# Performance work log

Hardware: AMD Instinct MI355X
Metric: run time of the kernel (lower is better)

The kernel has to match this reference:

```python
import jax, jax.numpy as jnp
import numpy as np

N_NODES = 100000
N_EDGES = 1600000
N_GRAPHS = 4096
GN_EPS = 1e-5
SLOPE = 0.01  # torch leaky_relu default negative_slope


def _graph_norm(x, w, b, s):
    # PyG GraphNorm with batch=None: single-graph normalization over all nodes
    mean = jnp.mean(x, axis=0, keepdims=True)
    out = x - s * mean
    var = jnp.mean(out * out, axis=0, keepdims=True)
    return w * out * jax.lax.rsqrt(var + GN_EPS) + b


def setup_inputs() -> dict:
    key = jax.random.key(0)
    ks = jax.random.split(key, 12)

    def rn(k, shape, fan_in):
        return (jax.random.normal(k, shape, jnp.float32) / np.float32(np.sqrt(fan_in)))

    return {
        "x": jax.random.normal(ks[0], (N_NODES, 48), jnp.float32),
        "edge_attr": jax.random.normal(ks[1], (N_EDGES, 10), jnp.float32),
        # GINConv MLP layer 0: Linear(48->128); layers 1..3: Linear(128->128)
        "W1_0": rn(ks[2], (48, 128), 48), "b1_0": jnp.zeros((128,), jnp.float32),
        "W1_rest": rn(ks[3], (3, 128, 128), 128), "b1_rest": jnp.zeros((3, 128), jnp.float32),
        # GraphNorm inside each MLP (weight, bias, mean_scale)
        "gn_w": jnp.ones((4, 128), jnp.float32), "gn_b": jnp.zeros((4, 128), jnp.float32), "gn_s": jnp.ones((4, 128), jnp.float32),
        # second Linear of each MLP (128->128; last conv maps to out_channels=128)
        "W2": rn(ks[4], (4, 128, 128), 128), "b2": jnp.zeros((4, 128), jnp.float32),
        # BasicGNN post-conv GraphNorms (after layers 0..2 only)
        "pn_w": jnp.ones((3, 128), jnp.float32), "pn_b": jnp.zeros((3, 128), jnp.float32), "pn_s": jnp.ones((3, 128), jnp.float32),
        # readout MLP head
        "fc1_W": rn(ks[5], (384, 64), 384), "fc1_b": jnp.zeros((64,), jnp.float32),
        "fc2_W": rn(ks[6], (64, 3), 64), "fc2_b": jnp.zeros((3,), jnp.float32),
        "edge_index": jax.random.randint(ks[7], (2, N_EDGES), 0, N_NODES),
        "batch": jnp.sort(jax.random.randint(ks[8], (N_NODES,), 0, N_GRAPHS)),
    }


def reference(x, edge_attr, W1_0, b1_0, W1_rest, b1_rest, gn_w, gn_b, gn_s,
              W2, b2, pn_w, pn_b, pn_s, fc1_W, fc1_b, fc2_W, fc2_b,
              edge_index, batch):
    # edge_attr is ignored: PyG GIN does not support edge attributes.
    src, dst = edge_index[0], edge_index[1]
    h = x
    for i in range(4):
        # GINConv: mlp((1+eps)*x_i + sum_{j in N(i)} x_j), eps = 0
        agg = jax.ops.segment_sum(h[src], dst, num_segments=N_NODES)
        m = h + agg
        if i == 0:
            m = m @ W1_0 + b1_0
        else:
            m = m @ W1_rest[i - 1] + b1_rest[i - 1]
        m = _graph_norm(m, gn_w[i], gn_b[i], gn_s[i])  # norm inside MLP
        m = jax.nn.leaky_relu(m, SLOPE)
        h = m @ W2[i] + b2[i]
        if i < 3:  # BasicGNN: norm + act after every conv except the last
            h = _graph_norm(h, pn_w[i], pn_b[i], pn_s[i])
            h = jax.nn.leaky_relu(h, SLOPE)

    # global mean / add / max pooling over data.batch
    sums = jax.ops.segment_sum(h, batch, num_segments=N_GRAPHS)
    cnt = jax.ops.segment_sum(jnp.ones((h.shape[0], 1), h.dtype), batch,
                              num_segments=N_GRAPHS)
    mean = sums / jnp.maximum(cnt, 1.0)
    mx = jax.ops.segment_max(h, batch, num_segments=N_GRAPHS)
    mx = jnp.where(jnp.isfinite(mx), mx, 0.0)  # guard empty segments

    g = jnp.concatenate([mean, sums, mx], axis=1)  # [G, 384]
    g = jax.nn.leaky_relu(g @ fc1_W + fc1_b, SLOPE)
    return g @ fc2_W + fc2_b  # [G, 3]
```

## Files before the change

kernel.cpp:

```cpp
#include <hip/hip_runtime.h>
#include <hip/hip_bf16.h>
#include <math.h>

#define N_NODES  100000
#define N_EDGES  1600000
#define N_GRAPHS 4096
#define NBUCKET  ((N_NODES + 127) / 128)
#define NPART    256
#define ROWBLKS_AL 6256

typedef __attribute__((ext_vector_type(4))) float f32x4;
typedef __attribute__((ext_vector_type(8))) short bf16x8;

__device__ __forceinline__ float lrelu(float x) { return fmaxf(x, 0.01f * x); }

__device__ __forceinline__ unsigned short f2bf(float f) {
    unsigned u = __float_as_uint(f);
    unsigned r = (u + 0x7FFFu + ((u >> 16) & 1u)) >> 16;
    return (unsigned short)r;
}
__device__ __forceinline__ float bf2f(unsigned short h) {
    return __uint_as_float(((unsigned)h) << 16);
}

__global__ __launch_bounds__(1024) void scan_kernel(const unsigned* __restrict__ in,
                                                    unsigned* __restrict__ out, int n) {
    __shared__ unsigned wsum[16];
    __shared__ unsigned carry_s;
    int t = threadIdx.x, lane = t & 63, wv = t >> 6;
    if (t == 0) carry_s = 0u;
    __syncthreads();
    for (int base = 0; base < n; base += 4096) {
        unsigned carry = carry_s;
        unsigned v[4]; unsigned s = 0u;
#pragma unroll
        for (int i = 0; i < 4; ++i) {
            int idx = base + t * 4 + i;
            v[i] = (idx < n) ? in[idx] : 0u;
            s += v[i];
        }
        unsigned ps = s;
#pragma unroll
        for (int off = 1; off < 64; off <<= 1) {
            unsigned x = __shfl_up(ps, off, 64);
            if (lane >= off) ps += x;
        }
        if (lane == 63) wsum[wv] = ps;
        __syncthreads();
        if (wv == 0 && lane < 16) {
            unsigned pw = wsum[lane];
#pragma unroll
            for (int off = 1; off < 16; off <<= 1) {
                unsigned x = __shfl_up(pw, off, 64);
                if (lane >= off) pw += x;
            }
            wsum[lane] = pw;
        }
        __syncthreads();
        unsigned wbase = wv ? wsum[wv - 1] : 0u;
        unsigned run = carry + wbase + (ps - s);
#pragma unroll
        for (int i = 0; i < 4; ++i) {
            int idx = base + t * 4 + i;
            if (idx < n) out[idx] = run;
            run += v[i];
        }
        unsigned total = wsum[15];
        __syncthreads();
        if (t == 0) carry_s = carry + total;
        __syncthreads();
    }
    if (t == 0) out[n] = carry_s;
}

__global__ __launch_bounds__(256) void phist_kernel(const int* __restrict__ dst,
        unsigned* __restrict__ cnt, int E, int chunk) {
    __shared__ unsigned lc[NBUCKET];
    int p = blockIdx.x, t = threadIdx.x;
    for (int i = t; i < NBUCKET; i += 256) lc[i] = 0u;
    __syncthreads();
    int e0 = p * chunk, e1 = e0 + chunk; if (e1 > E) e1 = E;
    for (int e = e0 + t; e < e1; e += 256)
        atomicAdd(&lc[((unsigned)dst[e]) >> 7], 1u);
    __syncthreads();
    for (int i = t; i < NBUCKET; i += 256) cnt[(size_t)p * NBUCKET + i] = lc[i];
}

__global__ void btot_kernel(const unsigned* __restrict__ cnt, unsigned* __restrict__ tot) {
    int b = blockIdx.x * 256 + threadIdx.x;
    if (b >= NBUCKET) return;
    unsigned s = 0u;
    for (int p = 0; p < NPART; ++p) s += cnt[(size_t)p * NBUCKET + b];
    tot[b] = s;
}

__global__ __launch_bounds__(256) void poff_kernel(unsigned* __restrict__ cnt,
        const unsigned* __restrict__ bucket_base) {
    int b = blockIdx.x * 4 + (threadIdx.x >> 6);
    if (b >= NBUCKET) return;
    int lane = threadIdx.x & 63;
    unsigned v[4]; unsigned s = 0u;
#pragma unroll
    for (int i = 0; i < 4; ++i) {
        int p = lane * 4 + i;
        v[i] = cnt[(size_t)p * NBUCKET + b];
        s += v[i];
    }
    unsigned ps = s;
#pragma unroll
    for (int off = 1; off < 64; off <<= 1) {
        unsigned x = __shfl_up(ps, off, 64);
        if (lane >= off) ps += x;
    }
    unsigned run = bucket_base[b] + (ps - s);
#pragma unroll
    for (int i = 0; i < 4; ++i) {
        int p = lane * 4 + i;
        cnt[(size_t)p * NBUCKET + b] = run;
        run += v[i];
    }
}

__global__ __launch_bounds__(256) void pscat_kernel(const int* __restrict__ ei,
        const unsigned* __restrict__ cnt, unsigned* __restrict__ pair, int E, int chunk) {
    __shared__ unsigned lcur[NBUCKET];
    int p = blockIdx.x, t = threadIdx.x;
    for (int i = t; i < NBUCKET; i += 256) lcur[i] = cnt[(size_t)p * NBUCKET + i];
    __syncthreads();
    int e0 = p * chunk, e1 = e0 + chunk; if (e1 > E) e1 = E;
    for (int e = e0 + t; e < e1; e += 256) {
        unsigned src = (unsigned)ei[e];
        unsigned dst = (unsigned)ei[E + e];
        unsigned b = dst >> 7;
        unsigned pos = atomicAdd(&lcur[b], 1u);
        pair[pos] = src | ((dst & 127u) << 20);
    }
}

__global__ __launch_bounds__(256) void fillc2_kernel(const unsigned* __restrict__ pair,
        const unsigned* __restrict__ bucket_base, unsigned* __restrict__ row_ptr,
        unsigned* __restrict__ col, int N) {
    __shared__ unsigned lcnt[128], lpre[128], lcur[128];
    int b = blockIdx.x;
    int node0 = b << 7;
    int t = threadIdx.x;
    if (t < 128) { lcnt[t] = 0u; lcur[t] = 0u; }
    __syncthreads();
    unsigned bb = bucket_base[b], be = bucket_base[b + 1];
    for (unsigned i = bb + t; i < be; i += 256)
        atomicAdd(&lcnt[(pair[i] >> 20) & 127u], 1u);
    __syncthreads();
    if (t < 64) {
        unsigned v0 = lcnt[2 * t], v1 = lcnt[2 * t + 1];
        unsigned s = v0 + v1;
        unsigned ps = s;
#pragma unroll
        for (int off = 1; off < 64; off <<= 1) {
            unsigned x = __shfl_up(ps, off, 64);
            if (t >= off) ps += x;
        }
        unsigned base = ps - s;
        lpre[2 * t] = base;
        lpre[2 * t + 1] = base + v0;
    }
    __syncthreads();
    if (t < 128) {
        int node = node0 + t;
        if (node < N) row_ptr[node] = bb + lpre[t];
    }
    if (b == (int)gridDim.x - 1 && t == 0) row_ptr[N] = be;
    for (unsigned i = bb + t; i < be; i += 256) {
        unsigned u = pair[i];
        unsigned d = (u >> 20) & 127u;
        unsigned pos = bb + lpre[d] + atomicAdd(&lcur[d], 1u);
        col[pos] = u & 0xFFFFFu;
    }
}

__global__ void gsearch_kernel(const int* __restrict__ batch, unsigned* __restrict__ gptr,
                               int N, int G) {
    int g = blockIdx.x * 256 + threadIdx.x;
    if (g > G) return;
    int lo = 0, hi = N;
    while (lo < hi) { int mid = (lo + hi) >> 1; if (batch[mid] < g) lo = mid + 1; else hi = mid; }
    gptr[g] = (unsigned)lo;
}

__global__ void cast_kernel(const float* __restrict__ in, unsigned short* __restrict__ outb, int n4) {
    int i = blockIdx.x * 256 + threadIdx.x;
    if (i >= n4) return;
    f32x4 v = *(const f32x4*)(in + (size_t)i * 4);
    uint2 u;
    u.x = (unsigned)f2bf(v[0]) | ((unsigned)f2bf(v[1]) << 16);
    u.y = (unsigned)f2bf(v[2]) | ((unsigned)f2bf(v[3]) << 16);
    *(uint2*)(outb + (size_t)i * 4) = u;
}

__global__ __launch_bounds__(256) void tfm_kernel(const unsigned short* __restrict__ hb,
        const float* __restrict__ stats, const float* __restrict__ wp,
        const float* __restrict__ bp, const float* __restrict__ sp, float invN,
        unsigned short* __restrict__ yb, int total8) {
    __shared__ float la[128], ldd[128];
    int t = threadIdx.x;
    if (t < 128) {
        float mean = stats[t] * invN;
        float ex2  = stats[128 + t] * invN;
        float sv   = sp[t];
        float var  = ex2 - 2.f * sv * mean * mean + sv * sv * mean * mean;
        float a    = wp[t] * rsqrtf(var + 1e-5f);
        la[t] = a; ldd[t] = bp[t] - a * sv * mean;
    }
    __syncthreads();
    int i = blockIdx.x * 256 + t;
    if (i >= total8) return;
    int c0 = (i & 15) * 8;
    uint4 u = *(const uint4*)(hb + (size_t)i * 8);
    unsigned uu[4] = {u.x, u.y, u.z, u.w};
    unsigned ow[4];
#pragma unroll
    for (int q = 0; q < 4; ++q) {
        int c = c0 + 2 * q;
        float v0 = lrelu(fmaf(la[c],     __uint_as_float(uu[q] << 16),         ldd[c]));
        float v1 = lrelu(fmaf(la[c + 1], __uint_as_float(uu[q] & 0xffff0000u), ldd[c + 1]));
        ow[q] = (unsigned)f2bf(v0) | ((unsigned)f2bf(v1) << 16);
    }
    uint4 o; o.x = ow[0]; o.y = ow[1]; o.z = ow[2]; o.w = ow[3];
    *(uint4*)(yb + (size_t)i * 8) = o;
}

template<int D, int KOCT>
__global__ __launch_bounds__(256) void agg_kernel(const unsigned short* __restrict__ hb, int ld_in,
        const unsigned* __restrict__ row_ptr, const unsigned* __restrict__ col,
        unsigned short* __restrict__ op, int n) {
    int node = blockIdx.x * 4 + (threadIdx.x >> 6);
    int l = threadIdx.x & 63;
    if (node >= n || l >= KOCT * 4) return;
    int c = 2 * l;
    float x0 = 0.f, x1 = 0.f;
    if (c < D) {
        const unsigned short* hp = hb + c;
#define LOADU(s) *(const unsigned*)(hp + (size_t)(s) * ld_in)
#define LO(u) __uint_as_float((u) << 16)
#define HI(u) __uint_as_float((u) & 0xffff0000u)
        unsigned su = LOADU(node);
        x0 = LO(su); x1 = HI(su);
        float y0 = 0.f, y1 = 0.f, z0 = 0.f, z1 = 0.f, q0 = 0.f, q1 = 0.f;
        unsigned e0 = row_ptr[node], e1 = row_ptr[node + 1];
        unsigned e = e0;
        for (; e + 8 <= e1; e += 8) {
            unsigned c0i = col[e],     c1i = col[e + 1], c2i = col[e + 2], c3i = col[e + 3];
            unsigned c4i = col[e + 4], c5i = col[e + 5], c6i = col[e + 6], c7i = col[e + 7];
            unsigned u0 = LOADU(c0i), u1 = LOADU(c1i), u2 = LOADU(c2i), u3 = LOADU(c3i);
            unsigned u4 = LOADU(c4i), u5 = LOADU(c5i), u6 = LOADU(c6i), u7 = LOADU(c7i);
            x0 += LO(u0); x1 += HI(u0); y0 += LO(u1); y1 += HI(u1);
            z0 += LO(u2); z1 += HI(u2); q0 += LO(u3); q1 += HI(u3);
            x0 += LO(u4); x1 += HI(u4); y0 += LO(u5); y1 += HI(u5);
            z0 += LO(u6); z1 += HI(u6); q0 += LO(u7); q1 += HI(u7);
        }
        for (; e + 4 <= e1; e += 4) {
            unsigned c0i = col[e], c1i = col[e + 1], c2i = col[e + 2], c3i = col[e + 3];
            unsigned u0 = LOADU(c0i), u1 = LOADU(c1i), u2 = LOADU(c2i), u3 = LOADU(c3i);
            x0 += LO(u0); x1 += HI(u0); y0 += LO(u1); y1 += HI(u1);
            z0 += LO(u2); z1 += HI(u2); q0 += LO(u3); q1 += HI(u3);
        }
        for (; e < e1; ++e) {
            unsigned u = LOADU(col[e]);
            x0 += LO(u); x1 += HI(u);
        }
#undef LOADU
#undef LO
#undef HI
        x0 = (x0 + y0) + (z0 + q0);
        x1 = (x1 + y1) + (z1 + q1);
    }
    unsigned outw = (unsigned)f2bf(x0) | ((unsigned)f2bf(x1) << 16);
    size_t fo = (((size_t)(node >> 4) * KOCT + (l >> 2)) * 16 + (node & 15)) * 8 + 2 * (l & 3);
    *(unsigned*)(op + fo) = outw;
}

__global__ __launch_bounds__(256) void wsplit_kernel(const float* __restrict__ W1_0,
        const float* __restrict__ W1_rest, const float* __restrict__ W2,
        unsigned short* __restrict__ wt) {
    int g = blockIdx.y;
    int i = blockIdx.x * 256 + threadIdx.x;
    int e = i & 7, lane = (i >> 3) & 63, h = (i >> 9) & 1, j = (i >> 10) & 7, ks = i >> 13;
    int m = lane & 15, kg = lane >> 4;
    int k = ks * 32 + kg * 8 + e;
    int n = 8 * m + j;
    float v = 0.f;
    if (g == 0) { if (k < 48) v = W1_0[k * 128 + n]; }
    else if (g & 1) v = W2[(size_t)((g - 1) >> 1) * 16384 + k * 128 + n];
    else            v = W1_rest[(size_t)((g - 2) >> 1) * 16384 + k * 128 + n];
    unsigned short hi = f2bf(v);
    unsigned short out = (h == 0) ? hi : f2bf(v - bf2f(hi));
    wt[(size_t)g * 32768 + i] = out;
}

template<int KS, int KOCT, bool AFF, bool STATS, bool BF16OUT, bool FRAGOUT>
__global__ __launch_bounds__(256, 2) void mgemm_kernel(
        const unsigned short* __restrict__ Ah,
        const float* __restrict__ stats, const float* __restrict__ wp,
        const float* __restrict__ bp, const float* __restrict__ sp, float invN,
        const unsigned short* __restrict__ Wt, const float* __restrict__ bias,
        unsigned short* __restrict__ outb, unsigned short* __restrict__ ofh,
        float* __restrict__ ostats, int M) {
    __shared__ float ls[256];
    int t = threadIdx.x;
    if (STATS) { ls[t] = 0.f; __syncthreads(); }
    int lane = t & 63;
    int m = lane & 15, kg = lane >> 4;
    int wid = t >> 6;
    int wr = wid >> 1, wc = wid & 1;
    int rowBase = blockIdx.x * 128 + wr * 64;
    int rowblk0 = blockIdx.x * 8 + wr * 4;

    union U8 { bf16x8 v; unsigned short u[8]; };

    f32x4 acc[4][4];
#pragma unroll
    for (int j = 0; j < 4; ++j) {
        float b = bias[8 * m + wc * 4 + j];
#pragma unroll
        for (int rg = 0; rg < 4; ++rg) acc[rg][j] = (f32x4){b, b, b, b};
    }

#pragma unroll
    for (int ks = 0; ks < KS; ++ks) {
        int k0 = ks * 32 + kg * 8;
        float aC[8], dC[8];
        if (AFF) {
            f32x4 sm0 = *(const f32x4*)(stats + k0),       sm1 = *(const f32x4*)(stats + k0 + 4);
            f32x4 se0 = *(const f32x4*)(stats + 128 + k0), se1 = *(const f32x4*)(stats + 128 + k0 + 4);
            f32x4 w0  = *(const f32x4*)(wp + k0),          w1  = *(const f32x4*)(wp + k0 + 4);
            f32x4 b0  = *(const f32x4*)(bp + k0),          b1  = *(const f32x4*)(bp + k0 + 4);
            f32x4 s0  = *(const f32x4*)(sp + k0),          s1  = *(const f32x4*)(sp + k0 + 4);
#pragma unroll
            for (int q = 0; q < 8; ++q) {
                float mean = (q < 4 ? sm0[q] : sm1[q - 4]) * invN;
                float ex2  = (q < 4 ? se0[q] : se1[q - 4]) * invN;
                float sv   = (q < 4 ? s0[q]  : s1[q - 4]);
                float var  = ex2 - 2.f * sv * mean * mean + sv * sv * mean * mean;
                float a    = (q < 4 ? w0[q] : w1[q - 4]) * rsqrtf(var + 1e-5f);
                aC[q] = a;
                dC[q] = (q < 4 ? b0[q] : b1[q - 4]) - a * sv * mean;
            }
        }
        U8 fh[4];
#pragma unroll
        for (int rg = 0; rg < 4; ++rg) {
            size_t ao = (((size_t)(rowblk0 + rg) * KOCT + ks * 4 + kg) << 7) + (m << 3);
            U8 h;
            h.v = *(const bf16x8*)(Ah + ao);
            if (AFF) {
#pragma unroll
                for (int q = 0; q < 8; ++q) {
                    float xv = lrelu(fmaf(aC[q], bf2f(h.u[q]), dC[q]));
                    h.u[q] = f2bf(xv);
                }
            }
            fh[rg] = h;
        }
#pragma unroll
        for (int j = 0; j < 4; ++j) {
            size_t wo = (size_t)(ks * 8 + wc * 4 + j) * 1024 + (size_t)lane * 8;
            bf16x8 whi = *(const bf16x8*)(Wt + wo);
            bf16x8 wlo = *(const bf16x8*)(Wt + wo + 512);
#pragma unroll
            for (int rg = 0; rg < 4; ++rg) {
                acc[rg][j] = __builtin_amdgcn_mfma_f32_16x16x32_bf16(fh[rg].v, whi, acc[rg][j], 0, 0, 0);
                acc[rg][j] = __builtin_amdgcn_mfma_f32_16x16x32_bf16(fh[rg].v, wlo, acc[rg][j], 0, 0, 0);
            }
        }
    }

#pragma unroll
    for (int rg = 0; rg < 4; ++rg) {
#pragma unroll
        for (int r = 0; r < 4; ++r) {
            int gr = rowBase + rg * 16 + kg * 4 + r;
            if (gr < M) {
                unsigned short h[4];
#pragma unroll
                for (int q = 0; q < 4; ++q) h[q] = f2bf(acc[rg][q][r]);
                uint2 uh;
                uh.x = (unsigned)h[0] | ((unsigned)h[1] << 16);
                uh.y = (unsigned)h[2] | ((unsigned)h[3] << 16);
                if (BF16OUT) *(uint2*)(outb + (size_t)gr * 128 + 8 * m + wc * 4) = uh;
                if (FRAGOUT) {
                    size_t fo = (((size_t)(rowblk0 + rg) * 16 + m) * 16 + (kg * 4 + r)) * 8 + wc * 4;
                    *(uint2*)(ofh + fo) = uh;
                }
            }
        }
    }

    if (STATS) {
#pragma unroll
        for (int j = 0; j < 4; ++j) {
            float s = 0.f, s2 = 0.f;
#pragma unroll
            for (int rg = 0; rg < 4; ++rg)
#pragma unroll
                for (int r = 0; r < 4; ++r) {
                    int gr = rowBase + rg * 16 + kg * 4 + r;
                    if (gr < M) { float v = acc[rg][j][r]; s += v; s2 += v * v; }
                }
            atomicAdd(&ls[8 * m + wc * 4 + j], s);
            atomicAdd(&ls[128 + 8 * m + wc * 4 + j], s2);
        }
        __syncthreads();
        atomicAdd(&ostats[t], ls[t]);
    }
}

__global__ __launch_bounds__(256) void pool_kernel(const unsigned short* __restrict__ hb,
        const unsigned* __restrict__ gptr, float* __restrict__ gout, int G) {
    int g = blockIdx.x * 4 + (threadIdx.x >> 6);
    int lane = threadIdx.x & 63;
    if (g >= G) return;
    unsigned s = gptr[g], e = gptr[g + 1];
    int c = 2 * lane;
    float sx = 0.f, sy = 0.f, mx = -INFINITY, my = -INFINITY;
    for (unsigned n = s; n < e; ++n) {
        unsigned u = *(const unsigned*)(hb + (size_t)n * 128 + c);
        float vx = __uint_as_float(u << 16);
        float vy = __uint_as_float(u & 0xffff0000u);
        sx += vx; sy += vy;
        mx = fmaxf(mx, vx); my = fmaxf(my, vy);
    }
    float cnt = (float)(e - s);
    float inv = 1.f / fmaxf(cnt, 1.f);
    if (e == s) { mx = 0.f; my = 0.f; }
    float* go = gout + (size_t)g * 384;
    go[c] = sx * inv;       go[c + 1] = sy * inv;
    go[128 + c] = sx;       go[128 + c + 1] = sy;
    go[256 + c] = mx;       go[256 + c + 1] = my;
}

__global__ __launch_bounds__(64) void head_kernel(const float* __restrict__ gbuf,
        const float* __restrict__ w1, const float* __restrict__ b1,
        const float* __restrict__ w2, const float* __restrict__ b2,
        float* __restrict__ out, int G) {
    __shared__ float y[64];
    int g = blockIdx.x, t = threadIdx.x;
    const float* row = gbuf + (size_t)g * 384;
    float acc = b1[t];
    for (int k = 0; k < 384; ++k) acc += row[k] * w1[(size_t)k * 64 + t];
    y[t] = lrelu(acc);
    __syncthreads();
    if (t < 3) {
        float o = b2[t];
        for (int k = 0; k < 64; ++k) o += y[k] * w2[k * 3 + t];
        out[(size_t)g * 3 + t] = o;
    }
}

extern "C" void kernel_launch(void* const* d_in, const int* in_sizes, int n_in,
                              void* d_out, int out_size, void* d_ws, size_t ws_size,
                              hipStream_t stream) {
    const float* x       = (const float*)d_in[0];
    const float* W1_0    = (const float*)d_in[2];
    const float* b1_0    = (const float*)d_in[3];
    const float* W1_rest = (const float*)d_in[4];
    const float* b1_rest = (const float*)d_in[5];
    const float* gn_w    = (const float*)d_in[6];
    const float* gn_b    = (const float*)d_in[7];
    const float* gn_s    = (const float*)d_in[8];
    const float* W2      = (const float*)d_in[9];
    const float* b2      = (const float*)d_in[10];
    const float* pn_w    = (const float*)d_in[11];
    const float* pn_b    = (const float*)d_in[12];
    const float* pn_s    = (const float*)d_in[13];
    const float* fc1W    = (const float*)d_in[14];
    const float* fc1b    = (const float*)d_in[15];
    const float* fc2W    = (const float*)d_in[16];
    const float* fc2b    = (const float*)d_in[17];
    const int*   ei      = (const int*)d_in[18];
    const int*   batch   = (const int*)d_in[19];
    float* outp = (float*)d_out;

    const int N = N_NODES, E = N_EDGES, G = N_GRAPHS;
    const int CHUNK = (E + NPART - 1) / NPART;
    const size_t FRAGSZ = (size_t)ROWBLKS_AL * 16 * 128;
    char* w = (char*)d_ws;
    auto alloc = [&](size_t bytes) -> char* {
        char* p = w; w += (bytes + 255) & ~(size_t)255; return p;
    };
    unsigned short* p1h = (unsigned short*)alloc(FRAGSZ * 2);
    unsigned short* p2h = (unsigned short*)alloc(FRAGSZ * 2);
    unsigned short* hb0 = (unsigned short*)alloc((size_t)N * 128 * 2);
    unsigned short* yb  = (unsigned short*)alloc((size_t)N * 128 * 2);
    unsigned short* xb  = (unsigned short*)alloc((size_t)N * 48 * 2);
    unsigned* row_ptr = (unsigned*)alloc((size_t)(N + 1) * 4);
    unsigned* colb    = (unsigned*)alloc((size_t)E * 4);
    unsigned* pair    = (unsigned*)alloc((size_t)E * 4);
    unsigned* cntm    = (unsigned*)alloc((size_t)NPART * NBUCKET * 4);
    unsigned* btot    = (unsigned*)alloc((size_t)(NBUCKET + 1) * 4);
    unsigned* bbase   = (unsigned*)alloc((size_t)(NBUCKET + 1) * 4);
    unsigned* gptr    = (unsigned*)alloc((size_t)(G + 1) * 4);
    float*    gbuf    = (float*)alloc((size_t)G * 384 * 4);
    unsigned short* wt = (unsigned short*)alloc((size_t)8 * 32768 * 2);
    float*    statsZ  = (float*)alloc(7 * 256 * 4);
    auto gnstats = [&](int i) { return statsZ + (size_t)i * 256; };
    auto pnstats = [&](int i) { return statsZ + (size_t)(4 + i) * 256; };

    hipMemsetAsync(statsZ, 0, 7 * 256 * 4, stream);

    phist_kernel<<<NPART, 256, 0, stream>>>(ei + E, cntm, E, CHUNK);
    btot_kernel<<<(NBUCKET + 255) / 256, 256, 0, stream>>>(cntm, btot);
    scan_kernel<<<1, 1024, 0, stream>>>(btot, bbase, NBUCKET);
    poff_kernel<<<(NBUCKET + 3) / 4, 256, 0, stream>>>(cntm, bbase);
    pscat_kernel<<<NPART, 256, 0, stream>>>(ei, cntm, pair, E, CHUNK);
    fillc2_kernel<<<NBUCKET, 256, 0, stream>>>(pair, bbase, row_ptr, colb, N);
    gsearch_kernel<<<(G + 256) / 256, 256, 0, stream>>>(batch, gptr, N, G);
    wsplit_kernel<<<dim3(128, 8), 256, 0, stream>>>(W1_0, W1_rest, W2, wt);
    cast_kernel<<<(N * 48 / 4 + 255) / 256, 256, 0, stream>>>(x, xb, N * 48 / 4);

    const float invN = 1.f / (float)N;
    int gemm_grid = (N + 127) / 128;
    int agg_grid  = (N + 3) / 4;
    int tfm_grid  = (N * 16 + 255) / 256;

    agg_kernel<48, 8><<<agg_grid, 256, 0, stream>>>(xb, 48, row_ptr, colb, p1h, N);
    mgemm_kernel<2, 8, false, true, false, true><<<gemm_grid, 256, 0, stream>>>(
            p1h, nullptr, nullptr, nullptr, nullptr, invN,
            wt, b1_0, nullptr, p2h, gnstats(0), N);
    mgemm_kernel<4, 16, true, true, true, false><<<gemm_grid, 256, 0, stream>>>(
            p2h, gnstats(0), gn_w, gn_b, gn_s, invN,
            wt + 1 * 32768, b2, hb0, nullptr, pnstats(0), N);

    for (int i = 1; i < 4; ++i) {
        tfm_kernel<<<tfm_grid, 256, 0, stream>>>(hb0, pnstats(i - 1),
                pn_w + (i - 1) * 128, pn_b + (i - 1) * 128, pn_s + (i - 1) * 128, invN,
                yb, N * 16);
        agg_kernel<128, 16><<<agg_grid, 256, 0, stream>>>(yb, 128, row_ptr, colb, p1h, N);
        mgemm_kernel<4, 16, false, true, false, true><<<gemm_grid, 256, 0, stream>>>(
                p1h, nullptr, nullptr, nullptr, nullptr, invN,
                wt + (size_t)(2 * i) * 32768, b1_rest + (size_t)(i - 1) * 128,
                nullptr, p2h, gnstats(i), N);
        if (i < 3) {
            mgemm_kernel<4, 16, true, true, true, false><<<gemm_grid, 256, 0, stream>>>(
                    p2h, gnstats(i), gn_w + i * 128, gn_b + i * 128, gn_s + i * 128, invN,
                    wt + (size_t)(2 * i + 1) * 32768, b2 + (size_t)i * 128,
                    hb0, nullptr, pnstats(i), N);
        } else {
            mgemm_kernel<4, 16, true, false, true, false><<<gemm_grid, 256, 0, stream>>>(
                    p2h, gnstats(3), gn_w + 3 * 128, gn_b + 3 * 128, gn_s + 3 * 128, invN,
                    wt + (size_t)7 * 32768, b2 + (size_t)3 * 128,
                    hb0, nullptr, nullptr, N);
        }
    }

    pool_kernel<<<(G + 3) / 4, 256, 0, stream>>>(hb0, gptr, gbuf, G);
    head_kernel<<<G, 64, 0, stream>>>(gbuf, fc1W, fc1b, fc2W, fc2b, outp, G);
}
```

Measured before the change: 705.4 us.

## Widen agg unroll to 16, raise gemm occupancy, fuse pooling with head

The neighbor-gather loop in the aggregation kernel now issues 16 column-index loads and 16 gathers per iteration instead of 8, to keep more memory requests in flight. The GEMM kernel's launch bounds ask for 3 blocks per CU instead of 2, which may force register spilling. Pooling and the readout MLP head are merged into one kernel that keeps the pooled vector in shared memory, removing a launch and the global round trip through gbuf.

```diff
diff --git a/kernel.cpp b/kernel.cpp
--- a/kernel.cpp
+++ b/kernel.cpp
@@ -247,15 +247,19 @@
         float y0 = 0.f, y1 = 0.f, z0 = 0.f, z1 = 0.f, q0 = 0.f, q1 = 0.f;
         unsigned e0 = row_ptr[node], e1 = row_ptr[node + 1];
         unsigned e = e0;
-        for (; e + 8 <= e1; e += 8) {
-            unsigned c0i = col[e],     c1i = col[e + 1], c2i = col[e + 2], c3i = col[e + 3];
-            unsigned c4i = col[e + 4], c5i = col[e + 5], c6i = col[e + 6], c7i = col[e + 7];
-            unsigned u0 = LOADU(c0i), u1 = LOADU(c1i), u2 = LOADU(c2i), u3 = LOADU(c3i);
-            unsigned u4 = LOADU(c4i), u5 = LOADU(c5i), u6 = LOADU(c6i), u7 = LOADU(c7i);
-            x0 += LO(u0); x1 += HI(u0); y0 += LO(u1); y1 += HI(u1);
-            z0 += LO(u2); z1 += HI(u2); q0 += LO(u3); q1 += HI(u3);
-            x0 += LO(u4); x1 += HI(u4); y0 += LO(u5); y1 += HI(u5);
-            z0 += LO(u6); z1 += HI(u6); q0 += LO(u7); q1 += HI(u7);
+        for (; e + 16 <= e1; e += 16) {
+            unsigned ci[16], ui[16];
+#pragma unroll
+            for (int k = 0; k < 16; ++k) ci[k] = col[e + k];
+#pragma unroll
+            for (int k = 0; k < 16; ++k) ui[k] = LOADU(ci[k]);
+#pragma unroll
+            for (int k = 0; k < 16; k += 4) {
+                x0 += LO(ui[k]);     x1 += HI(ui[k]);
+                y0 += LO(ui[k + 1]); y1 += HI(ui[k + 1]);
+                z0 += LO(ui[k + 2]); z1 += HI(ui[k + 2]);
+                q0 += LO(ui[k + 3]); q1 += HI(ui[k + 3]);
+            }
         }
         for (; e + 4 <= e1; e += 4) {
             unsigned c0i = col[e], c1i = col[e + 1], c2i = col[e + 2], c3i = col[e + 3];
@@ -297,7 +301,7 @@
 }
 
 template<int KS, int KOCT, bool AFF, bool STATS, bool BF16OUT, bool FRAGOUT>
-__global__ __launch_bounds__(256, 2) void mgemm_kernel(
+__global__ __launch_bounds__(256, 3) void mgemm_kernel(
         const unsigned short* __restrict__ Ah,
         const float* __restrict__ stats, const float* __restrict__ wp,
         const float* __restrict__ bp, const float* __restrict__ sp, float invN,
@@ -413,13 +417,16 @@
     }
 }
 
-__global__ __launch_bounds__(256) void pool_kernel(const unsigned short* __restrict__ hb,
-        const unsigned* __restrict__ gptr, float* __restrict__ gout, int G) {
-    int g = blockIdx.x * 4 + (threadIdx.x >> 6);
-    int lane = threadIdx.x & 63;
-    if (g >= G) return;
+__global__ __launch_bounds__(64) void poolhead_kernel(const unsigned short* __restrict__ hb,
+        const unsigned* __restrict__ gptr,
+        const float* __restrict__ w1, const float* __restrict__ b1,
+        const float* __restrict__ w2, const float* __restrict__ b2,
+        float* __restrict__ out, int G) {
+    __shared__ float red[384];
+    __shared__ float y[64];
+    int g = blockIdx.x, t = threadIdx.x;
     unsigned s = gptr[g], e = gptr[g + 1];
-    int c = 2 * lane;
+    int c = 2 * t;
     float sx = 0.f, sy = 0.f, mx = -INFINITY, my = -INFINITY;
     for (unsigned n = s; n < e; ++n) {
         unsigned u = *(const unsigned*)(hb + (size_t)n * 128 + c);
@@ -431,21 +438,12 @@
     float cnt = (float)(e - s);
     float inv = 1.f / fmaxf(cnt, 1.f);
     if (e == s) { mx = 0.f; my = 0.f; }
-    float* go = gout + (size_t)g * 384;
-    go[c] = sx * inv;       go[c + 1] = sy * inv;
-    go[128 + c] = sx;       go[128 + c + 1] = sy;
-    go[256 + c] = mx;       go[256 + c + 1] = my;
-}
-
-__global__ __launch_bounds__(64) void head_kernel(const float* __restrict__ gbuf,
-        const float* __restrict__ w1, const float* __restrict__ b1,
-        const float* __restrict__ w2, const float* __restrict__ b2,
-        float* __restrict__ out, int G) {
-    __shared__ float y[64];
-    int g = blockIdx.x, t = threadIdx.x;
-    const float* row = gbuf + (size_t)g * 384;
+    red[c] = sx * inv;   red[c + 1] = sy * inv;
+    red[128 + c] = sx;   red[129 + c] = sy;
+    red[256 + c] = mx;   red[257 + c] = my;
+    __syncthreads();
     float acc = b1[t];
-    for (int k = 0; k < 384; ++k) acc += row[k] * w1[(size_t)k * 64 + t];
+    for (int k = 0; k < 384; ++k) acc += red[k] * w1[(size_t)k * 64 + t];
     y[t] = lrelu(acc);
     __syncthreads();
     if (t < 3) {
@@ -498,7 +496,6 @@
     unsigned* btot    = (unsigned*)alloc((size_t)(NBUCKET + 1) * 4);
     unsigned* bbase   = (unsigned*)alloc((size_t)(NBUCKET + 1) * 4);
     unsigned* gptr    = (unsigned*)alloc((size_t)(G + 1) * 4);
-    float*    gbuf    = (float*)alloc((size_t)G * 384 * 4);
     unsigned short* wt = (unsigned short*)alloc((size_t)8 * 32768 * 2);
     float*    statsZ  = (float*)alloc(7 * 256 * 4);
     auto gnstats = [&](int i) { return statsZ + (size_t)i * 256; };
@@ -551,6 +548,5 @@
         }
     }
 
-    pool_kernel<<<(G + 3) / 4, 256, 0, stream>>>(hb0, gptr, gbuf, G);
-    head_kernel<<<G, 64, 0, stream>>>(gbuf, fc1W, fc1b, fc2W, fc2b, outp, G);
-}
+    poolhead_kernel<<<G, 64, 0, stream>>>(hb0, gptr, fc1W, fc1b, fc2W, fc2b, outp, G);
+}
```

Result: no change. 711.8 us (+0.9%).
